# Performance work log

Measured on AMD Instinct MI355X. Metric: run time of the kernel, lower is better.

The kernel has to match this reference:

```python
import jax, jax.numpy as jnp
import numpy as np


def _prelu(x, a):
    return jnp.where(x >= 0, x, a * x)


def _conv1x1(x, w, b, a):
    # x: (B,C,H,W), w: (O,C), b: (O,), a: PReLU scalar (shared, torch default)
    y = jnp.einsum('bchw,oc->bohw', x, w) + b[None, :, None, None]
    return _prelu(y, a)


def setup_inputs() -> dict:
    key = jax.random.key(0)
    ks = jax.random.split(key, 7)
    B, C, H, W = 8, 128, 256, 256
    std = 1.0 / np.sqrt(C)
    x = jax.random.normal(ks[0], (B, C, H, W), dtype=jnp.float32)
    Wf = jax.random.normal(ks[1], (C, C), dtype=jnp.float32) * std
    bf = jax.random.normal(ks[2], (C,), dtype=jnp.float32) * std
    Wg = jax.random.normal(ks[3], (C, C), dtype=jnp.float32) * std
    bg = jax.random.normal(ks[4], (C,), dtype=jnp.float32) * std
    Wh = jax.random.normal(ks[5], (C, C), dtype=jnp.float32) * std
    bh = jax.random.normal(ks[6], (C,), dtype=jnp.float32) * std
    af = jnp.float32(0.25)
    ag = jnp.float32(0.25)
    ah = jnp.float32(0.25)
    return {"x": x, "Wf": Wf, "bf": bf, "af": af,
            "Wg": Wg, "bg": bg, "ag": ag,
            "Wh": Wh, "bh": bh, "ah": ah}


def reference(x, Wf, bf, af, Wg, bg, ag, Wh, bh, ah):
    # 1x1 conv projections + PReLU
    map_f = _conv1x1(x, Wf, bf, af)          # (B,C,H,W)
    map_g = _conv1x1(x, Wg, bg, ag)          # (B,C,H,W)
    map_h = _conv1x1(x, Wh, bh, ah)          # (B,C,H,W)
    # map_f.transpose(2,3) @ map_g -> (B,C,W,W), unscaled single-head attention
    atten = jnp.einsum('bchw,bchv->bcwv', map_f, map_g)  # (B,C,W,W)
    atten = jax.nn.softmax(atten, axis=-1)
    # map_h @ atten -> (B,C,H,W)
    out = jnp.einsum('bchw,bcwv->bchv', map_h, atten)
    return out + x
```

## Files before the change

### kernel.cpp

```cpp
#include <hip/hip_runtime.h>

typedef __bf16 bf16_t;
typedef __bf16 bf16x8 __attribute__((ext_vector_type(8)));
typedef __bf16 bf16x4 __attribute__((ext_vector_type(4)));
typedef float  f32x4  __attribute__((ext_vector_type(4)));

#define HW_ 65536
#define C_  128

__device__ __forceinline__ int swz(int r) { return ((r ^ (r >> 3)) & 7) << 4; }

#define LGKM0() asm volatile("s_waitcnt lgkmcnt(0)" ::: "memory")
__device__ __forceinline__ void BAR() {
  asm volatile("" ::: "memory");
  __builtin_amdgcn_s_barrier();
  asm volatile("" ::: "memory");
}

template<bool HBLK>
__device__ __forceinline__ void conv_one(char* lds, const float* __restrict__ Wsrc,
                                         const float* __restrict__ bias, float alpha,
                                         bf16_t* __restrict__ dst, size_t pb,
                                         int wv, int lr, int lq, int t, int s0)
{
  __syncthreads();
  #pragma unroll
  for (int rep = 0; rep < 16; ++rep) {
    int q = rep * 256 + t;
    int o = q >> 5, c0 = (q & 31) * 4;
    f32x4 w4 = *(const f32x4*)(Wsrc + o * C_ + c0);
    bf16x4 v;
    v[0] = (bf16_t)w4[0]; v[1] = (bf16_t)w4[1]; v[2] = (bf16_t)w4[2]; v[3] = (bf16_t)w4[3];
    *(bf16x4*)(lds + 32768 + ((o * 256 + c0 * 2) ^ swz(o))) = v;
  }
  __syncthreads();

  const f32x4 fz = {0.f, 0.f, 0.f, 0.f};
  f32x4 acc[2][8];
  #pragma unroll
  for (int mf = 0; mf < 2; ++mf)
    #pragma unroll
    for (int nf = 0; nf < 8; ++nf)
      acc[mf][nf] = fz;

  #pragma unroll
  for (int ks = 0; ks < 4; ++ks) {
    int kb = ks * 32 + lq * 8;
    bf16x8 a[2], bb[8];
    #pragma unroll
    for (int mf = 0; mf < 2; ++mf) {
      int m = wv * 32 + mf * 16 + lr;
      a[mf] = *(const bf16x8*)(lds + 32768 + ((m * 256 + kb * 2) ^ swz(m)));
    }
    #pragma unroll
    for (int nf = 0; nf < 8; ++nf) {
      int n = nf * 16 + lr;
      bb[nf] = *(const bf16x8*)(lds + ((n * 256 + kb * 2) ^ swz(n)));
    }
    #pragma unroll
    for (int mf = 0; mf < 2; ++mf)
      #pragma unroll
      for (int nf = 0; nf < 8; ++nf)
        acc[mf][nf] = __builtin_amdgcn_mfma_f32_16x16x32_bf16(a[mf], bb[nf], acc[mf][nf], 0, 0, 0);
  }

  #pragma unroll
  for (int mf = 0; mf < 2; ++mf) {
    #pragma unroll
    for (int i = 0; i < 4; ++i) {
      int o = wv * 32 + mf * 16 + lq * 4 + i;
      float bo = bias[o];
      #pragma unroll
      for (int nf = 0; nf < 8; ++nf) {
        int s = s0 + nf * 16 + lr;
        float v = acc[mf][nf][i] + bo;
        v = (v >= 0.f) ? v : alpha * v;
        size_t off;
        if (HBLK) {
          int h = s >> 8, w = s & 255;
          off = pb + (size_t)o * HW_ + (size_t)(w >> 5) * 8192 + h * 32 + (w & 31);
        } else {
          off = pb + (size_t)o * HW_ + s;
        }
        dst[off] = (bf16_t)v;
      }
    }
  }
}

__global__ __launch_bounds__(256, 2) void conv_kernel(
    const float* __restrict__ x,
    const float* __restrict__ Wf, const float* __restrict__ bfp, const float* __restrict__ afp,
    const float* __restrict__ Wg, const float* __restrict__ bgp, const float* __restrict__ agp,
    const float* __restrict__ Wh, const float* __restrict__ bhp, const float* __restrict__ ahp,
    bf16_t* __restrict__ mF, bf16_t* __restrict__ mG, bf16_t* __restrict__ mH, int b0)
{
  __shared__ __align__(16) char lds[65536];
  const int t = threadIdx.x;
  const int bloc = blockIdx.y;
  const int s0 = blockIdx.x * 128;
  const size_t xbase = ((size_t)(b0 + bloc) * C_) * HW_ + s0;

  #pragma unroll
  for (int rep = 0; rep < 4; ++rep) {
    int q = rep * 256 + t;
    int c0 = (q >> 5) * 4, sl0 = (q & 31) * 4;
    f32x4 r[4];
    #pragma unroll
    for (int i = 0; i < 4; ++i)
      r[i] = *(const f32x4*)(x + xbase + (size_t)(c0 + i) * HW_ + sl0);
    #pragma unroll
    for (int js = 0; js < 4; ++js) {
      int s = sl0 + js;
      bf16x4 v;
      v[0] = (bf16_t)r[0][js]; v[1] = (bf16_t)r[1][js];
      v[2] = (bf16_t)r[2][js]; v[3] = (bf16_t)r[3][js];
      *(bf16x4*)(lds + ((s * 256 + c0 * 2) ^ swz(s))) = v;
    }
  }

  const int wv = t >> 6, lane = t & 63, lr = lane & 15, lq = lane >> 4;
  const size_t pb = (size_t)bloc * C_ * HW_;
  conv_one<false>(lds, Wf, bfp, afp[0], mF, pb, wv, lr, lq, t, s0);
  conv_one<false>(lds, Wg, bgp, agp[0], mG, pb, wv, lr, lq, t, s0);
  conv_one<true >(lds, Wh, bhp, ahp[0], mH, pb, wv, lr, lq, t, s0);
}

#define SMAX_OFF 131072
#define SSUM_OFF 133120
#define ATTN_SMEM 135168

__global__ __launch_bounds__(512, 2) void attn_kernel(
    const bf16_t* __restrict__ mF, const bf16_t* __restrict__ mG, const bf16_t* __restrict__ mH,
    const float* __restrict__ x, float* __restrict__ out, int b0)
{
  extern __shared__ __align__(16) char smem[];
  const int t = threadIdx.x;
  const int c = blockIdx.x, bloc = blockIdx.y;
  const int lane = t & 63, lr = lane & 15, lq = lane >> 4;
  const int wv = t >> 6, wr = wv >> 1, wc = wv & 1;
  const size_t plane  = ((size_t)bloc * C_ + c) * HW_;
  const size_t gplane = (((size_t)(b0 + bloc)) * C_ + c) * HW_;

  const f32x4 fz = {0.f, 0.f, 0.f, 0.f};
  f32x4 acc[4][8];
  #pragma unroll
  for (int mf = 0; mf < 4; ++mf)
    #pragma unroll
    for (int nf = 0; nf < 8; ++nf)
      acc[mf][nf] = fz;

  const int hq = t >> 5, wb8 = t & 31;

  bf16x8 pfF[4], pfG[4];
  #pragma unroll
  for (int i = 0; i < 4; ++i) {
    pfF[i] = *(const bf16x8*)(mF + plane + (size_t)(hq * 4 + i) * 256 + wb8 * 8);
    pfG[i] = *(const bf16x8*)(mG + plane + (size_t)(hq * 4 + i) * 256 + wb8 * 8);
  }

  #pragma unroll
  for (int hb = 0; hb < 256; hb += 64) {
    #pragma unroll
    for (int j = 0; j < 8; ++j) {
      int w = wb8 * 8 + j;
      bf16x4 v; v[0] = pfF[0][j]; v[1] = pfF[1][j]; v[2] = pfF[2][j]; v[3] = pfF[3][j];
      *(bf16x4*)(smem + ((w * 128 + hq * 8) ^ swz(w))) = v;
      bf16x4 g; g[0] = pfG[0][j]; g[1] = pfG[1][j]; g[2] = pfG[2][j]; g[3] = pfG[3][j];
      *(bf16x4*)(smem + 32768 + ((w * 128 + hq * 8) ^ swz(w))) = g;
    }
    if (hb < 192) {
      #pragma unroll
      for (int i = 0; i < 4; ++i) {
        pfF[i] = *(const bf16x8*)(mF + plane + (size_t)(hb + 64 + hq * 4 + i) * 256 + wb8 * 8);
        pfG[i] = *(const bf16x8*)(mG + plane + (size_t)(hb + 64 + hq * 4 + i) * 256 + wb8 * 8);
      }
    }
    LGKM0(); BAR();
    #pragma unroll
    for (int k0 = 0; k0 < 64; k0 += 32) {
      const int kb = k0 + lq * 8;
      bf16x8 af[4], bq[8];
      #pragma unroll
      for (int mf = 0; mf < 4; ++mf) {
        int m = wr * 64 + mf * 16 + lr;
        af[mf] = *(const bf16x8*)(smem + ((m * 128 + kb * 2) ^ swz(m)));
      }
      #pragma unroll
      for (int nf = 0; nf < 8; ++nf) {
        int n = wc * 128 + nf * 16 + lr;
        bq[nf] = *(const bf16x8*)(smem + 32768 + ((n * 128 + kb * 2) ^ swz(n)));
      }
      #pragma unroll
      for (int mf = 0; mf < 4; ++mf)
        #pragma unroll
        for (int nf = 0; nf < 8; ++nf)
          acc[mf][nf] = __builtin_amdgcn_mfma_f32_16x16x32_bf16(af[mf], bq[nf], acc[mf][nf], 0, 0, 0);
    }
    BAR();
  }

  float* smax = (float*)(smem + SMAX_OFF);
  float* ssum = (float*)(smem + SSUM_OFF);
  float rowm[4][4];
  #pragma unroll
  for (int mf = 0; mf < 4; ++mf)
    #pragma unroll
    for (int i = 0; i < 4; ++i) {
      float m = acc[mf][0][i];
      #pragma unroll
      for (int nf = 1; nf < 8; ++nf) m = fmaxf(m, acc[mf][nf][i]);
      #pragma unroll
      for (int d = 1; d < 16; d <<= 1) m = fmaxf(m, __shfl_xor(m, d));
      rowm[mf][i] = m;
    }
  if (lr == 0) {
    #pragma unroll
    for (int mf = 0; mf < 4; ++mf)
      #pragma unroll
      for (int i = 0; i < 4; ++i)
        smax[wc * 256 + wr * 64 + mf * 16 + lq * 4 + i] = rowm[mf][i];
  }
  LGKM0(); BAR();
  float m2[4][4], rs[4][4];
  #pragma unroll
  for (int mf = 0; mf < 4; ++mf)
    #pragma unroll
    for (int i = 0; i < 4; ++i) {
      int w = wr * 64 + mf * 16 + lq * 4 + i;
      m2[mf][i] = fmaxf(smax[w], smax[256 + w]);
      rs[mf][i] = 0.f;
    }
  #pragma unroll
  for (int mf = 0; mf < 4; ++mf)
    #pragma unroll
    for (int nf = 0; nf < 8; ++nf)
      #pragma unroll
      for (int i = 0; i < 4; ++i) {
        float e = __expf(acc[mf][nf][i] - m2[mf][i]);
        acc[mf][nf][i] = e;
        rs[mf][i] += e;
      }
  #pragma unroll
  for (int mf = 0; mf < 4; ++mf)
    #pragma unroll
    for (int i = 0; i < 4; ++i) {
      float s = rs[mf][i];
      #pragma unroll
      for (int d = 1; d < 16; d <<= 1) s += __shfl_xor(s, d);
      rs[mf][i] = s;
    }
  if (lr == 0) {
    #pragma unroll
    for (int mf = 0; mf < 4; ++mf)
      #pragma unroll
      for (int i = 0; i < 4; ++i)
        ssum[wc * 256 + wr * 64 + mf * 16 + lq * 4 + i] = rs[mf][i];
  }
  LGKM0(); BAR();

  #pragma unroll
  for (int mf = 0; mf < 4; ++mf) {
    float rinv[4];
    #pragma unroll
    for (int i = 0; i < 4; ++i) {
      int w = wr * 64 + mf * 16 + lq * 4 + i;
      rinv[i] = 1.f / (ssum[w] + ssum[256 + w]);
    }
    int wpb = (wr * 64 + mf * 16 + lq * 4) * 2;
    #pragma unroll
    for (int nf = 0; nf < 8; ++nf) {
      int v_ = wc * 128 + nf * 16 + lr;
      bf16x4 v;
      #pragma unroll
      for (int i = 0; i < 4; ++i) v[i] = (bf16_t)(acc[mf][nf][i] * rinv[i]);
      *(bf16x4*)(smem + ((v_ * 512 + wpb) ^ swz(v_))) = v;
    }
  }

  const bf16_t* hp = mH + plane;
  bf16x8 aP[3][2];
  #pragma unroll
  for (int p = 0; p < 3; ++p)
    #pragma unroll
    for (int mf = 0; mf < 2; ++mf) {
      int h = wv * 32 + mf * 16 + lr;
      aP[p][mf] = *(const bf16x8*)(hp + (size_t)p * 8192 + h * 32 + lq * 8);
    }

  LGKM0(); BAR();

  f32x4 oac[2][16];
  #pragma unroll
  for (int mf = 0; mf < 2; ++mf)
    #pragma unroll
    for (int nf = 0; nf < 16; ++nf)
      oac[mf][nf] = fz;

  __builtin_amdgcn_s_setprio(1);
  #pragma unroll
  for (int kc = 0; kc < 8; ++kc) {
    bf16x8 a0 = aP[kc % 3][0], a1 = aP[kc % 3][1];
    if (kc < 5) {
      #pragma unroll
      for (int mf = 0; mf < 2; ++mf) {
        int h = wv * 32 + mf * 16 + lr;
        aP[kc % 3][mf] = *(const bf16x8*)(hp + (size_t)(kc + 3) * 8192 + h * 32 + lq * 8);
      }
    }
    #pragma unroll
    for (int nf = 0; nf < 16; ++nf) {
      int v_ = nf * 16 + lr;
      bf16x8 bq = *(const bf16x8*)(smem + ((v_ * 512 + kc * 64 + lq * 16) ^ swz(v_)));
      oac[0][nf] = __builtin_amdgcn_mfma_f32_16x16x32_bf16(a0, bq, oac[0][nf], 0, 0, 0);
      oac[1][nf] = __builtin_amdgcn_mfma_f32_16x16x32_bf16(a1, bq, oac[1][nf], 0, 0, 0);
    }
  }
  __builtin_amdgcn_s_setprio(0);

  #pragma unroll
  for (int mf = 0; mf < 2; ++mf)
    #pragma unroll
    for (int i = 0; i < 4; ++i) {
      int h = wv * 32 + mf * 16 + lq * 4 + i;
      #pragma unroll
      for (int nf = 0; nf < 16; ++nf) {
        int v_ = nf * 16 + lr;
        size_t off = gplane + (size_t)h * 256 + v_;
        out[off] = oac[mf][nf][i] + x[off];
      }
    }
}

extern "C" void kernel_launch(void* const* d_in, const int* in_sizes, int n_in,
                              void* d_out, int out_size, void* d_ws, size_t ws_size,
                              hipStream_t stream)
{
  (void)in_sizes; (void)n_in; (void)out_size;
  const float* x   = (const float*)d_in[0];
  const float* Wf  = (const float*)d_in[1];
  const float* bfp = (const float*)d_in[2];
  const float* afp = (const float*)d_in[3];
  const float* Wg  = (const float*)d_in[4];
  const float* bgp = (const float*)d_in[5];
  const float* agp = (const float*)d_in[6];
  const float* Wh  = (const float*)d_in[7];
  const float* bhp = (const float*)d_in[8];
  const float* ahp = (const float*)d_in[9];
  float* out = (float*)d_out;

  const size_t per_map_b = (size_t)C_ * HW_ * sizeof(bf16_t);
  int nb = 1;
  if      (ws_size >= 3 * 8 * per_map_b) nb = 8;
  else if (ws_size >= 3 * 4 * per_map_b) nb = 4;
  else if (ws_size >= 3 * 2 * per_map_b) nb = 2;

  hipFuncSetAttribute(reinterpret_cast<const void*>(attn_kernel),
                      hipFuncAttributeMaxDynamicSharedMemorySize, ATTN_SMEM);

  bf16_t* mF = (bf16_t*)d_ws;
  bf16_t* mG = mF + (size_t)nb * C_ * HW_;
  bf16_t* mH = mG + (size_t)nb * C_ * HW_;

  for (int b0 = 0; b0 < 8; b0 += nb) {
    conv_kernel<<<dim3(512, nb), 256, 0, stream>>>(x, Wf, bfp, afp, Wg, bgp, agp,
                                                   Wh, bhp, ahp, mF, mG, mH, b0);
    attn_kernel<<<dim3(C_, nb), 512, ATTN_SMEM, stream>>>(mF, mG, mH, x, out, b0);
  }
}
```

Baseline: 434.5 us.

## Store F/G maps transposed from conv and load attention operands directly from global

The conv kernel now tiles spatially as 8h x 16w blocks and writes the F and G maps transposed (w-major, h contiguous) with 16-byte vector stores. This lets the attention kernel read MFMA operands straight from global memory, double-buffered in registers, instead of transposing through LDS with barriers. It removes the LDS staging and the syncs in the first GEMM, and turns scalar bf16 stores into vector stores. The cost is direct global/L2 reads per wave with more register pressure, and the conv input loads become less contiguous (16-wide rows).

```diff
diff --git a/kernel.cpp b/kernel.cpp
--- a/kernel.cpp
+++ b/kernel.cpp
@@ -21,7 +21,7 @@
 __device__ __forceinline__ void conv_one(char* lds, const float* __restrict__ Wsrc,
                                          const float* __restrict__ bias, float alpha,
                                          bf16_t* __restrict__ dst, size_t pb,
-                                         int wv, int lr, int lq, int t, int s0)
+                                         int wv, int lr, int lq, int t, int h0, int w0)
 {
   __syncthreads();
   #pragma unroll
@@ -70,19 +70,22 @@
     for (int i = 0; i < 4; ++i) {
       int o = wv * 32 + mf * 16 + lq * 4 + i;
       float bo = bias[o];
-      #pragma unroll
-      for (int nf = 0; nf < 8; ++nf) {
-        int s = s0 + nf * 16 + lr;
-        float v = acc[mf][nf][i] + bo;
-        v = (v >= 0.f) ? v : alpha * v;
-        size_t off;
-        if (HBLK) {
-          int h = s >> 8, w = s & 255;
-          off = pb + (size_t)o * HW_ + (size_t)(w >> 5) * 8192 + h * 32 + (w & 31);
-        } else {
-          off = pb + (size_t)o * HW_ + s;
+      if (!HBLK) {
+        bf16x8 v8;
+        #pragma unroll
+        for (int nf = 0; nf < 8; ++nf) {
+          float v = acc[mf][nf][i] + bo;
+          v8[nf] = (bf16_t)((v >= 0.f) ? v : alpha * v);
         }
-        dst[off] = (bf16_t)v;
+        *(bf16x8*)(dst + pb + (size_t)o * HW_ + (size_t)(w0 + lr) * 256 + h0) = v8;
+      } else {
+        int w = w0 + lr;
+        size_t base = pb + (size_t)o * HW_ + (size_t)(w >> 5) * 8192 + (w & 31);
+        #pragma unroll
+        for (int nf = 0; nf < 8; ++nf) {
+          float v = acc[mf][nf][i] + bo;
+          dst[base + (size_t)(h0 + nf) * 32] = (bf16_t)((v >= 0.f) ? v : alpha * v);
+        }
       }
     }
   }
@@ -97,33 +100,35 @@
 {
   __shared__ __align__(16) char lds[65536];
   const int t = threadIdx.x;
-  const int bloc = blockIdx.y;
-  const int s0 = blockIdx.x * 128;
-  const size_t xbase = ((size_t)(b0 + bloc) * C_) * HW_ + s0;
+  const int h0 = blockIdx.x * 8;
+  const int w0 = blockIdx.y * 16;
+  const int bloc = blockIdx.z;
+  const size_t xbase = ((size_t)(b0 + bloc) * C_) * HW_;
 
   #pragma unroll
   for (int rep = 0; rep < 4; ++rep) {
     int q = rep * 256 + t;
-    int c0 = (q >> 5) * 4, sl0 = (q & 31) * 4;
+    int wq = q & 3, hl = (q >> 2) & 7, c0 = (q >> 5) * 4;
     f32x4 r[4];
     #pragma unroll
     for (int i = 0; i < 4; ++i)
-      r[i] = *(const f32x4*)(x + xbase + (size_t)(c0 + i) * HW_ + sl0);
-    #pragma unroll
-    for (int js = 0; js < 4; ++js) {
-      int s = sl0 + js;
+      r[i] = *(const f32x4*)(x + xbase + (size_t)(c0 + i) * HW_
+                             + (size_t)(h0 + hl) * 256 + w0 + wq * 4);
+    #pragma unroll
+    for (int j = 0; j < 4; ++j) {
+      int s = hl * 16 + wq * 4 + j;
       bf16x4 v;
-      v[0] = (bf16_t)r[0][js]; v[1] = (bf16_t)r[1][js];
-      v[2] = (bf16_t)r[2][js]; v[3] = (bf16_t)r[3][js];
+      v[0] = (bf16_t)r[0][j]; v[1] = (bf16_t)r[1][j];
+      v[2] = (bf16_t)r[2][j]; v[3] = (bf16_t)r[3][j];
       *(bf16x4*)(lds + ((s * 256 + c0 * 2) ^ swz(s))) = v;
     }
   }
 
   const int wv = t >> 6, lane = t & 63, lr = lane & 15, lq = lane >> 4;
   const size_t pb = (size_t)bloc * C_ * HW_;
-  conv_one<false>(lds, Wf, bfp, afp[0], mF, pb, wv, lr, lq, t, s0);
-  conv_one<false>(lds, Wg, bgp, agp[0], mG, pb, wv, lr, lq, t, s0);
-  conv_one<true >(lds, Wh, bhp, ahp[0], mH, pb, wv, lr, lq, t, s0);
+  conv_one<false>(lds, Wf, bfp, afp[0], mF, pb, wv, lr, lq, t, h0, w0);
+  conv_one<false>(lds, Wg, bgp, agp[0], mG, pb, wv, lr, lq, t, h0, w0);
+  conv_one<true >(lds, Wh, bhp, ahp[0], mH, pb, wv, lr, lq, t, h0, w0);
 }
 
 #define SMAX_OFF 131072
@@ -150,55 +155,48 @@
     for (int nf = 0; nf < 8; ++nf)
       acc[mf][nf] = fz;
 
-  const int hq = t >> 5, wb8 = t & 31;
-
-  bf16x8 pfF[4], pfG[4];
-  #pragma unroll
-  for (int i = 0; i < 4; ++i) {
-    pfF[i] = *(const bf16x8*)(mF + plane + (size_t)(hq * 4 + i) * 256 + wb8 * 8);
-    pfG[i] = *(const bf16x8*)(mG + plane + (size_t)(hq * 4 + i) * 256 + wb8 * 8);
-  }
-
-  #pragma unroll
-  for (int hb = 0; hb < 256; hb += 64) {
-    #pragma unroll
-    for (int j = 0; j < 8; ++j) {
-      int w = wb8 * 8 + j;
-      bf16x4 v; v[0] = pfF[0][j]; v[1] = pfF[1][j]; v[2] = pfF[2][j]; v[3] = pfF[3][j];
-      *(bf16x4*)(smem + ((w * 128 + hq * 8) ^ swz(w))) = v;
-      bf16x4 g; g[0] = pfG[0][j]; g[1] = pfG[1][j]; g[2] = pfG[2][j]; g[3] = pfG[3][j];
-      *(bf16x4*)(smem + 32768 + ((w * 128 + hq * 8) ^ swz(w))) = g;
-    }
-    if (hb < 192) {
-      #pragma unroll
-      for (int i = 0; i < 4; ++i) {
-        pfF[i] = *(const bf16x8*)(mF + plane + (size_t)(hb + 64 + hq * 4 + i) * 256 + wb8 * 8);
-        pfG[i] = *(const bf16x8*)(mG + plane + (size_t)(hb + 64 + hq * 4 + i) * 256 + wb8 * 8);
-      }
-    }
-    LGKM0(); BAR();
-    #pragma unroll
-    for (int k0 = 0; k0 < 64; k0 += 32) {
-      const int kb = k0 + lq * 8;
-      bf16x8 af[4], bq[8];
-      #pragma unroll
-      for (int mf = 0; mf < 4; ++mf) {
-        int m = wr * 64 + mf * 16 + lr;
-        af[mf] = *(const bf16x8*)(smem + ((m * 128 + kb * 2) ^ swz(m)));
-      }
-      #pragma unroll
-      for (int nf = 0; nf < 8; ++nf) {
-        int n = wc * 128 + nf * 16 + lr;
-        bq[nf] = *(const bf16x8*)(smem + 32768 + ((n * 128 + kb * 2) ^ swz(n)));
-      }
-      #pragma unroll
-      for (int mf = 0; mf < 4; ++mf)
-        #pragma unroll
-        for (int nf = 0; nf < 8; ++nf)
-          acc[mf][nf] = __builtin_amdgcn_mfma_f32_16x16x32_bf16(af[mf], bq[nf], acc[mf][nf], 0, 0, 0);
-    }
-    BAR();
-  }
+  const bf16_t* fp = mF + plane;
+  const bf16_t* gp = mG + plane;
+  const int ko = lq * 8;
+
+#define S_LOAD(AF, BQ, KB)                                                   \
+  {                                                                          \
+    _Pragma("unroll")                                                        \
+    for (int mf = 0; mf < 4; ++mf) {                                         \
+      int m = wr * 64 + mf * 16 + lr;                                        \
+      AF[mf] = *(const bf16x8*)(fp + (size_t)m * 256 + (KB) + ko);           \
+    }                                                                        \
+    _Pragma("unroll")                                                        \
+    for (int nf = 0; nf < 8; ++nf) {                                         \
+      int n = wc * 128 + nf * 16 + lr;                                       \
+      BQ[nf] = *(const bf16x8*)(gp + (size_t)n * 256 + (KB) + ko);           \
+    }                                                                        \
+  }
+#define S_MFMA(AF, BQ)                                                       \
+  {                                                                          \
+    _Pragma("unroll")                                                        \
+    for (int mf = 0; mf < 4; ++mf)                                           \
+      _Pragma("unroll")                                                      \
+      for (int nf = 0; nf < 8; ++nf)                                         \
+        acc[mf][nf] = __builtin_amdgcn_mfma_f32_16x16x32_bf16(AF[mf], BQ[nf], acc[mf][nf], 0, 0, 0); \
+  }
+
+  {
+    bf16x8 afA[4], bqA[8], afB[4], bqB[8];
+    S_LOAD(afA, bqA, 0)
+    #pragma unroll
+    for (int ks = 0; ks < 8; ++ks) {
+      if ((ks & 1) == 0) {
+        if (ks < 7) S_LOAD(afB, bqB, (ks + 1) * 32)
+        S_MFMA(afA, bqA)
+      } else {
+        if (ks < 7) S_LOAD(afA, bqA, (ks + 1) * 32)
+        S_MFMA(afB, bqB)
+      }
+    }
+  }
+#undef S_LOAD
+#undef S_MFMA
 
   float* smax = (float*)(smem + SMAX_OFF);
   float* ssum = (float*)(smem + SSUM_OFF);
@@ -363,8 +361,8 @@
   bf16_t* mH = mG + (size_t)nb * C_ * HW_;
 
   for (int b0 = 0; b0 < 8; b0 += nb) {
-    conv_kernel<<<dim3(512, nb), 256, 0, stream>>>(x, Wf, bfp, afp, Wg, bgp, agp,
-                                                   Wh, bhp, ahp, mF, mG, mH, b0);
+    conv_kernel<<<dim3(32, 16, nb), 256, 0, stream>>>(x, Wf, bfp, afp, Wg, bgp, agp,
+                                                      Wh, bhp, ahp, mF, mG, mH, b0);
     attn_kernel<<<dim3(C_, nb), 512, ATTN_SMEM, stream>>>(mF, mG, mH, x, out, b0);
   }
 }
```

New measurement: 620.4 us. 1.43x slower.
